# Optimization experiments

Measured on AMD Instinct MI355X. Metric: run time of the kernel, lower is better.

## Reference

```python
import jax, jax.numpy as jnp
import numpy as np

B, T, S, D, H, DK = 2, 2048, 2048, 1024, 16, 64


def setup_inputs() -> dict:
    key = jax.random.key(0)
    ks = jax.random.split(key, 11)
    s = 1.0 / np.sqrt(D)
    return {
        "query": jax.random.normal(ks[0], (B, T, D), jnp.float32),
        "value": jax.random.normal(ks[1], (B, S, D), jnp.float32),
        "key": jax.random.normal(ks[2], (B, S, D), jnp.float32),
        "Wq": jax.random.normal(ks[3], (D, H, DK), jnp.float32) * s,
        "bq": jnp.zeros((H, DK), jnp.float32),
        "Wk": jax.random.normal(ks[4], (D, H, DK), jnp.float32) * s,
        "bk": jnp.zeros((H, DK), jnp.float32),
        "Wv": jax.random.normal(ks[5], (D, H, DK), jnp.float32) * s,
        "bv": jnp.zeros((H, DK), jnp.float32),
        "Wo": jax.random.normal(ks[6], (H, DK, D), jnp.float32) * (1.0 / np.sqrt(H * DK)),
        "bo": jnp.zeros((D,), jnp.float32),
    }


def reference(query, value, key, Wq, bq, Wk, bk, Wv, bv, Wo, bo):
    # Projections: (B, seq, D) x (D, H, DK) -> (B, seq, H, DK)
    q = jnp.einsum("btd,dhk->bthk", query, Wq) + bq
    k = jnp.einsum("bsd,dhk->bshk", key, Wk) + bk
    v = jnp.einsum("bsd,dhk->bshk", value, Wv) + bv
    # Scaled dot-product attention (keras scales query by 1/sqrt(key_dim))
    q = q * (1.0 / np.sqrt(DK)).astype(np.float32)
    scores = jnp.einsum("bshk,bthk->bhts", k, q)  # (B, H, T, S)
    probs = jax.nn.softmax(scores, axis=-1)
    attn = jnp.einsum("bhts,bshk->bthk", probs, v)  # (B, T, H, DK)
    # Output projection back to model dim
    out = jnp.einsum("bthk,hkd->btd", attn, Wo) + bo
    return out
```

## Files before the change

kernel.cpp:

```cpp
#include <hip/hip_runtime.h>
#include <math.h>

#define BB  2
#define TT  2048
#define SSQ 2048
#define DD  1024
#define HH  16
#define DKK 64
#define MM  (BB*TT)
#define NN  (HH*DKK)

typedef __attribute__((ext_vector_type(8))) short short8;
typedef __attribute__((ext_vector_type(4))) float f32x4;
typedef __attribute__((ext_vector_type(2))) unsigned int uint2v;
typedef __attribute__((ext_vector_type(4))) unsigned int u32x4;

__device__ __forceinline__ short f2bf(float x) {
    unsigned u = __builtin_bit_cast(unsigned, x);
    unsigned r = (u + 0x7FFFu + ((u >> 16) & 1u)) >> 16;
    return (short)r;
}

__device__ __forceinline__ unsigned pk2(float lo, float hi) {
    return (__builtin_bit_cast(unsigned, hi) & 0xFFFF0000u) |
           (__builtin_bit_cast(unsigned, lo) >> 16);
}

__device__ __forceinline__ short8 cvt8(f32x4 x, f32x4 y) {
    unsigned r0, r1, r2, r3;
    asm("v_cvt_pk_bf16_f32 %0, %1, %2" : "=v"(r0) : "v"(x[0]), "v"(x[1]));
    asm("v_cvt_pk_bf16_f32 %0, %1, %2" : "=v"(r1) : "v"(x[2]), "v"(x[3]));
    asm("v_cvt_pk_bf16_f32 %0, %1, %2" : "=v"(r2) : "v"(y[0]), "v"(y[1]));
    asm("v_cvt_pk_bf16_f32 %0, %1, %2" : "=v"(r3) : "v"(y[2]), "v"(y[3]));
    u32x4 r;
    r[0] = r0; r[1] = r1; r[2] = r2; r[3] = r3;
    return __builtin_bit_cast(short8, r);
}

__device__ __forceinline__ void glds16(const void* g, void* l) {
    __builtin_amdgcn_global_load_lds(
        (const __attribute__((address_space(1))) void*)g,
        (__attribute__((address_space(3))) void*)l, 16, 0, 0);
}

__global__ __launch_bounds__(256)
void wtrans(const float* __restrict__ w0, const float* __restrict__ w1,
            const float* __restrict__ w2, const float* __restrict__ w3,
            short* __restrict__ t0, short* __restrict__ t1,
            short* __restrict__ t2, short* __restrict__ t3)
{
    __shared__ float Ls[64][65];
    int z = blockIdx.z;
    const float* in = (z == 0) ? w0 : (z == 1) ? w1 : (z == 2) ? w2 : w3;
    short* out = (z == 0) ? t0 : (z == 1) ? t1 : (z == 2) ? t2 : t3;
    const int r0 = blockIdx.y * 64, c0 = blockIdx.x * 64;
    const int t = threadIdx.x;
    const int r = t >> 2, c4 = t & 3;

    const float* src = in + (size_t)(r0 + r) * DD + c0 + c4 * 16;
#pragma unroll
    for (int i = 0; i < 4; i++) {
        f32x4 f = *(const f32x4*)(src + i * 4);
#pragma unroll
        for (int j = 0; j < 4; j++) Ls[r][c4 * 16 + i * 4 + j] = f[j];
    }
    __syncthreads();

    short8 va, vb;
#pragma unroll
    for (int j = 0; j < 8; j++) va[j] = f2bf(Ls[c4 * 16 + j][r]);
#pragma unroll
    for (int j = 0; j < 8; j++) vb[j] = f2bf(Ls[c4 * 16 + 8 + j][r]);
    short* dst = out + (size_t)(c0 + r) * DD + r0 + c4 * 16;
    *(short8*)dst = va;
    *(short8*)(dst + 8) = vb;
}

__global__ __launch_bounds__(256, 3)
void gemm_qkv(const float* __restrict__ Aqf, const float* __restrict__ Akf,
              const float* __restrict__ Avf,
              const short* __restrict__ Wqt, const short* __restrict__ Wkt,
              const short* __restrict__ Wvt,
              const float* __restrict__ bq, const float* __restrict__ bk,
              const float* __restrict__ bv,
              short* __restrict__ Qb, short* __restrict__ Kb,
              short* __restrict__ Vbt)
{
    __shared__ short As[2][128 * 32];
    __shared__ short Bs[2][128 * 32];

    const int d = blockIdx.x + 8 * blockIdx.y + 256 * blockIdx.z;
    const int kx = d & 7, j = d >> 3;
    const int z = j >> 5;
    const int n0 = ((j >> 2) & 7) * 128;
    const int m0 = (4 * kx + (j & 3)) * 128;

    const float* A  = (z == 0) ? Aqf : (z == 1) ? Akf : Avf;
    const short* Bt = (z == 0) ? Wqt : (z == 1) ? Wkt : Wvt;
    const float* bias = (z == 0) ? bq : (z == 1) ? bk : bv;

    const int tid = threadIdx.x;
    const int w = tid >> 6, l = tid & 63;
    const int l15 = l & 15, quad = l >> 4;
    const int wm = w >> 1, wn = w & 1;
    const int r = tid >> 2, cseg = tid & 3;

    f32x4 acc[4][4];
#pragma unroll
    for (int i = 0; i < 4; i++)
#pragma unroll
        for (int jj = 0; jj < 4; jj++) acc[i][jj] = (f32x4){0.f, 0.f, 0.f, 0.f};

    const float* gA0 = A + (size_t)(m0 + r) * DD + cseg * 8;
    const float* gA1 = gA0 + (size_t)64 * DD;
    const short* gB  = Bt + (size_t)(n0 + r) * DD + cseg * 8;
    const int aoff0 = r * 32 + cseg * 8;
    const int aoff1 = (64 + r) * 32 + cseg * 8;

    glds16(gB + 0,                &Bs[0][w * 512]);
    glds16(gB + (size_t)64 * DD,  &Bs[0][2048 + w * 512]);
    {
        f32x4 a00 = *(const f32x4*)(gA0);
        f32x4 a01 = *(const f32x4*)(gA0 + 4);
        f32x4 a10 = *(const f32x4*)(gA1);
        f32x4 a11 = *(const f32x4*)(gA1 + 4);
        *(short8*)&As[0][aoff0] = cvt8(a00, a01);
        *(short8*)&As[0][aoff1] = cvt8(a10, a11);
    }

    for (int k0 = 0; k0 < DD; k0 += 32) {
        const int cur = (k0 >> 5) & 1;
        __syncthreads();
        const bool more = (k0 + 32) < DD;
        f32x4 a00, a01, a10, a11;
        if (more) {
            glds16(gB + k0 + 32,                  &Bs[cur ^ 1][w * 512]);
            glds16(gB + (size_t)64 * DD + k0 + 32, &Bs[cur ^ 1][2048 + w * 512]);
            a00 = *(const f32x4*)(gA0 + k0 + 32);
            a01 = *(const f32x4*)(gA0 + k0 + 36);
            a10 = *(const f32x4*)(gA1 + k0 + 32);
            a11 = *(const f32x4*)(gA1 + k0 + 36);
        }

        short8 bF[4];
#pragma unroll
        for (int ni = 0; ni < 4; ni++)
            bF[ni] = *(const short8*)&Bs[cur][(wn * 64 + ni * 16 + l15) * 32 + quad * 8];
        if (z != 2) {
#pragma unroll
            for (int mi = 0; mi < 4; mi++) {
                short8 aF = *(const short8*)&As[cur][(wm * 64 + mi * 16 + l15) * 32 + quad * 8];
#pragma unroll
                for (int ni = 0; ni < 4; ni++)
                    acc[mi][ni] = __builtin_amdgcn_mfma_f32_16x16x32_bf16(aF, bF[ni], acc[mi][ni], 0, 0, 0);
            }
        } else {
#pragma unroll
            for (int mi = 0; mi < 4; mi++) {
                short8 aF = *(const short8*)&As[cur][(wm * 64 + mi * 16 + l15) * 32 + quad * 8];
#pragma unroll
                for (int ni = 0; ni < 4; ni++)
                    acc[ni][mi] = __builtin_amdgcn_mfma_f32_16x16x32_bf16(bF[ni], aF, acc[ni][mi], 0, 0, 0);
            }
        }

        if (more) {
            *(short8*)&As[cur ^ 1][aoff0] = cvt8(a00, a01);
            *(short8*)&As[cur ^ 1][aoff1] = cvt8(a10, a11);
        }
    }

    if (z != 2) {
        short* dst = (z == 0) ? Qb : Kb;
        const float scale = (z == 0) ? 0.1803368801f : 1.0f;
#pragma unroll
        for (int mi = 0; mi < 4; mi++) {
#pragma unroll
            for (int reg = 0; reg < 4; reg++) {
                int m = m0 + wm * 64 + mi * 16 + quad * 4 + reg;
                int b = m >> 11, t = m & 2047;
#pragma unroll
                for (int ni = 0; ni < 4; ni++) {
                    int n = n0 + wn * 64 + ni * 16 + l15;
                    float vv = (acc[mi][ni][reg] + bias[n]) * scale;
                    int h = n >> 6, dk = n & 63;
                    dst[((size_t)(b * HH + h) * TT + t) * DKK + dk] = f2bf(vv);
                }
            }
        }
    } else {
        const int b = m0 >> 11;
        const int tl0 = (m0 & 2047) + wm * 64;
#pragma unroll
        for (int ni = 0; ni < 4; ni++) {
#pragma unroll
            for (int reg = 0; reg < 4; reg++) {
                int n = n0 + wn * 64 + ni * 16 + quad * 4 + reg;
                int h = n >> 6, dk = n & 63;
                float bb = bias[n];
                short* vrow = Vbt + ((size_t)(b * HH + h) * DKK + dk) * SSQ;
#pragma unroll
                for (int mi = 0; mi < 4; mi++) {
                    int t = tl0 + mi * 16 + l15;
                    vrow[t] = f2bf(acc[ni][mi][reg] + bb);
                }
            }
        }
    }
}

__global__ __launch_bounds__(256, 3)
void gemm_out(const short* __restrict__ Ab, const short* __restrict__ Wot,
              const float* __restrict__ bo, float* __restrict__ out)
{
    __shared__ short As[2][64 * 32];
    __shared__ short Bs[2][128 * 32];

    const int d = blockIdx.x + 8 * blockIdx.y;
    const int kx = d & 7, j = d >> 3;
    const int m0 = (8 * kx + (j & 7)) * 64;
    const int n0 = (j >> 3) * 128;

    const int tid = threadIdx.x;
    const int w = tid >> 6, l = tid & 63;
    const int l15 = l & 15, quad = l >> 4;
    const int wm = w >> 1, wn = w & 1;

    f32x4 acc[2][4];
#pragma unroll
    for (int i = 0; i < 2; i++)
#pragma unroll
        for (int jj = 0; jj < 4; jj++) acc[i][jj] = (f32x4){0.f, 0.f, 0.f, 0.f};

    const int r = tid >> 2, cseg = tid & 3;
    const short* gA = Ab + (size_t)(m0 + r) * DD + cseg * 8;
    const short* gB = Wot + (size_t)(n0 + r) * DD + cseg * 8;

    glds16(gA + 0,               &As[0][w * 512]);
    glds16(gB + 0,               &Bs[0][w * 512]);
    glds16(gB + (size_t)64 * DD, &Bs[0][2048 + w * 512]);

    for (int k0 = 0; k0 < DD; k0 += 32) {
        const int cur = (k0 >> 5) & 1;
        __syncthreads();
        if (k0 + 32 < DD) {
            glds16(gA + k0 + 32,                   &As[cur ^ 1][w * 512]);
            glds16(gB + k0 + 32,                   &Bs[cur ^ 1][w * 512]);
            glds16(gB + (size_t)64 * DD + k0 + 32, &Bs[cur ^ 1][2048 + w * 512]);
        }

        short8 bF[4];
#pragma unroll
        for (int ni = 0; ni < 4; ni++)
            bF[ni] = *(const short8*)&Bs[cur][(wn * 64 + ni * 16 + l15) * 32 + quad * 8];
#pragma unroll
        for (int mi = 0; mi < 2; mi++) {
            short8 aF = *(const short8*)&As[cur][(wm * 32 + mi * 16 + l15) * 32 + quad * 8];
#pragma unroll
            for (int ni = 0; ni < 4; ni++)
                acc[mi][ni] = __builtin_amdgcn_mfma_f32_16x16x32_bf16(aF, bF[ni], acc[mi][ni], 0, 0, 0);
        }
    }

#pragma unroll
    for (int mi = 0; mi < 2; mi++) {
#pragma unroll
        for (int reg = 0; reg < 4; reg++) {
            int m = m0 + wm * 32 + mi * 16 + quad * 4 + reg;
#pragma unroll
            for (int ni = 0; ni < 4; ni++) {
                int n = n0 + wn * 64 + ni * 16 + l15;
                out[(size_t)m * DD + n] = acc[mi][ni][reg] + bo[n];
            }
        }
    }
}

__global__ __launch_bounds__(256, 4)
void attn_mfma(const short* __restrict__ Qb, const short* __restrict__ Kb,
               const short* __restrict__ Vbt,
               float* __restrict__ O1, float* __restrict__ O2,
               float* __restrict__ l1, float* __restrict__ l2)
{
    __shared__ short KV[2 * 2 * 64 * 72];

    const int tid = threadIdx.x;
    const int w = tid >> 6, l = tid & 63;
    const int l15 = l & 15, quad = l >> 4;

    const int fid = blockIdx.y * 16 + blockIdx.x;
    const int swz = (fid & 7) * 64 + (fid >> 3);
    const int t0 = (swz & 15) * 128;
    const int bh = swz >> 4;
    const int half = blockIdx.z;
    const size_t hb = (size_t)bh * SSQ * DKK;
    const int r = tid >> 2, c4 = tid & 3;
    const int sbase = half * 1024;

    short8 qf[2][2];
#pragma unroll
    for (int mf = 0; mf < 2; mf++)
#pragma unroll
        for (int kk = 0; kk < 2; kk++)
            qf[mf][kk] = *(const short8*)(Qb + hb +
                (size_t)(t0 + 32 * w + 16 * mf + l15) * DKK + kk * 32 + quad * 8);

    const short* gkb = Kb + hb + (size_t)(sbase + r) * DKK + c4 * 16;
    const short* gvb = Vbt + hb + (size_t)r * SSQ + sbase + c4 * 16;
    short8 kr0 = *(const short8*)(gkb + 0);
    short8 kr1 = *(const short8*)(gkb + 8);
    short8 vr0 = *(const short8*)(gvb + 0);
    short8 vr1 = *(const short8*)(gvb + 8);

    f32x4 o[2][4];
#pragma unroll
    for (int mf = 0; mf < 2; mf++)
#pragma unroll
        for (int j = 0; j < 4; j++) o[mf][j] = (f32x4){0.f, 0.f, 0.f, 0.f};
    f32x4 lacc[2] = {(f32x4){0.f, 0.f, 0.f, 0.f}, (f32x4){0.f, 0.f, 0.f, 0.f}};
    const short8 ones = {(short)0x3F80, (short)0x3F80, (short)0x3F80, (short)0x3F80,
                         (short)0x3F80, (short)0x3F80, (short)0x3F80, (short)0x3F80};

    short* skb = KV + r * 72 + c4 * 16;

    for (int s0 = 0; s0 < 1024; s0 += 64) {
        const int dbo = (s0 & 64) ? 9216 : 0;
        *(short8*)(skb + dbo)          = kr0;
        *(short8*)(skb + dbo + 8)      = kr1;
        *(short8*)(skb + dbo + 4608)   = vr0;
        *(short8*)(skb + dbo + 4616)   = vr1;
        if (s0 + 64 < 1024) {
            const short* gk = gkb + (size_t)(s0 + 64) * DKK;
            const short* gv = gvb + (s0 + 64);
            kr0 = *(const short8*)(gk + 0);
            kr1 = *(const short8*)(gk + 8);
            vr0 = *(const short8*)(gv + 0);
            vr1 = *(const short8*)(gv + 8);
        }
        __syncthreads();
        const short* kb_ = KV + dbo;
        const short* vb_ = kb_ + 4608;

        f32x4 sc[4][2];
#pragma unroll
        for (int np = 0; np < 4; np++)
#pragma unroll
            for (int mf = 0; mf < 2; mf++) sc[np][mf] = (f32x4){0.f, 0.f, 0.f, 0.f};
        __builtin_amdgcn_s_setprio(1);
#pragma unroll
        for (int kk = 0; kk < 2; kk++) {
#pragma unroll
            for (int np = 0; np < 4; np++) {
                short8 aK = *(const short8*)&kb_[(16 * np + l15) * 72 + kk * 32 + quad * 8];
                sc[np][0] = __builtin_amdgcn_mfma_f32_16x16x32_bf16(aK, qf[0][kk], sc[np][0], 0, 0, 0);
                sc[np][1] = __builtin_amdgcn_mfma_f32_16x16x32_bf16(aK, qf[1][kk], sc[np][1], 0, 0, 0);
            }
        }
        __builtin_amdgcn_s_setprio(0);

        short8 pa[2][2];
#pragma unroll
        for (int mf = 0; mf < 2; mf++) {
#pragma unroll
            for (int kk = 0; kk < 2; kk++) {
                u32x4 wd;
#pragma unroll
                for (int b = 0; b < 2; b++) {
                    float p00 = __builtin_amdgcn_exp2f(sc[2 * kk][mf][2 * b]);
                    float p01 = __builtin_amdgcn_exp2f(sc[2 * kk][mf][2 * b + 1]);
                    float p10 = __builtin_amdgcn_exp2f(sc[2 * kk + 1][mf][2 * b]);
                    float p11 = __builtin_amdgcn_exp2f(sc[2 * kk + 1][mf][2 * b + 1]);
                    unsigned Xw = pk2(p00, p01);
                    unsigned Yw = pk2(p10, p11);
                    uint2v s1 = __builtin_amdgcn_permlane32_swap(Xw, Yw, false, false);
                    uint2v s2 = __builtin_amdgcn_permlane16_swap(s1[0], s1[1], false, false);
                    wd[b]     = s2[0];
                    wd[2 + b] = s2[1];
                }
                pa[mf][kk] = __builtin_bit_cast(short8, wd);
            }
        }

        __builtin_amdgcn_s_setprio(1);
#pragma unroll
        for (int kk = 0; kk < 2; kk++) {
            lacc[0] = __builtin_amdgcn_mfma_f32_16x16x32_bf16(pa[0][kk], ones, lacc[0], 0, 0, 0);
            lacc[1] = __builtin_amdgcn_mfma_f32_16x16x32_bf16(pa[1][kk], ones, lacc[1], 0, 0, 0);
#pragma unroll
            for (int np = 0; np < 4; np++) {
                short8 bV = *(const short8*)&vb_[(16 * np + l15) * 72 + kk * 32 + quad * 8];
                o[0][np] = __builtin_amdgcn_mfma_f32_16x16x32_bf16(pa[0][kk], bV, o[0][np], 0, 0, 0);
                o[1][np] = __builtin_amdgcn_mfma_f32_16x16x32_bf16(pa[1][kk], bV, o[1][np], 0, 0, 0);
            }
        }
        __builtin_amdgcn_s_setprio(0);
    }

    float* O = half ? O2 : O1;
    float* L = half ? l2 : l1;
    const size_t rowb = (size_t)bh * TT;
#pragma unroll
    for (int mf = 0; mf < 2; mf++) {
#pragma unroll
        for (int reg = 0; reg < 4; reg++) {
            int t = t0 + 32 * w + 16 * mf + quad * 4 + reg;
            if (l15 == 0) L[rowb + t] = lacc[mf][reg];
            float* orow = O + (rowb + t) * DKK;
#pragma unroll
            for (int np = 0; np < 4; np++)
                orow[16 * np + l15] = o[mf][np][reg];
        }
    }
}

__global__ __launch_bounds__(256)
void combine_norm(const float* __restrict__ O1, const float* __restrict__ O2,
                  const float* __restrict__ l1, const float* __restrict__ l2,
                  short* __restrict__ Ab)
{
    size_t g = (size_t)blockIdx.x * 256 + threadIdx.x;
    size_t i0 = g * 8;
    int bh = (int)(i0 >> 17);
    int t  = (int)((i0 >> 6) & 2047);
    int dk = (int)(i0 & 63);
    float inv = 1.f / (l1[(size_t)bh * TT + t] + l2[(size_t)bh * TT + t]);
    f32x4 a0 = *(const f32x4*)(O1 + i0);
    f32x4 a1 = *(const f32x4*)(O1 + i0 + 4);
    f32x4 b0 = *(const f32x4*)(O2 + i0);
    f32x4 b1 = *(const f32x4*)(O2 + i0 + 4);
    short8 v;
#pragma unroll
    for (int j = 0; j < 4; j++) v[j] = f2bf((a0[j] + b0[j]) * inv);
#pragma unroll
    for (int j = 0; j < 4; j++) v[4 + j] = f2bf((a1[j] + b1[j]) * inv);
    int b = bh >> 4, h = bh & 15;
    *(short8*)(Ab + (((size_t)(b * TT + t) * HH + h) * DKK + dk)) = v;
}

extern "C" void kernel_launch(void* const* d_in, const int* in_sizes, int n_in,
                              void* d_out, int out_size, void* d_ws, size_t ws_size,
                              hipStream_t stream)
{
    const float* query = (const float*)d_in[0];
    const float* value = (const float*)d_in[1];
    const float* key   = (const float*)d_in[2];
    const float* Wq    = (const float*)d_in[3];
    const float* bq    = (const float*)d_in[4];
    const float* Wk    = (const float*)d_in[5];
    const float* bk    = (const float*)d_in[6];
    const float* Wv    = (const float*)d_in[7];
    const float* bv    = (const float*)d_in[8];
    const float* Wo    = (const float*)d_in[9];
    const float* bo    = (const float*)d_in[10];
    float* out = (float*)d_out;

    const size_t actE = (size_t)MM * DD;
    const size_t wE   = (size_t)DD * NN;
    short* p = (short*)d_ws;
    short* Wqt  = p; p += wE;
    short* Wkt  = p; p += wE;
    short* Wvt  = p; p += wE;
    short* Wot  = p; p += wE;
    short* Qb   = p; p += actE;
    short* Kb   = p; p += actE;
    short* Vbt  = p; p += actE;
    short* Ab   = p; p += actE;
    float* O1f  = (float*)p; p += 2 * actE;
    float* O2f  = (float*)p; p += 2 * actE;
    float* l1f  = (float*)p; p += 4 * (size_t)BB * HH * TT;
    float* l2f  = l1f + (size_t)BB * HH * TT;

    dim3 blk(256);

    wtrans<<<dim3(16, 16, 4), blk, 0, stream>>>(Wq, Wk, Wv, Wo, Wqt, Wkt, Wvt, Wot);

    gemm_qkv<<<dim3(NN / 128, MM / 128, 3), blk, 0, stream>>>(
        query, key, value, Wqt, Wkt, Wvt, bq, bk, bv, Qb, Kb, Vbt);

    attn_mfma<<<dim3(TT / 128, BB * HH, 2), blk, 0, stream>>>(
        Qb, Kb, Vbt, O1f, O2f, l1f, l2f);

    combine_norm<<<dim3((unsigned)(actE / 2048)), blk, 0, stream>>>(
        O1f, O2f, l1f, l2f, Ab);

    gemm_out<<<dim3(NN / 128, MM / 64), blk, 0, stream>>>(Ab, Wot, bo, out);
}
```

Before: 249.1 us.

## Pre-convert activations to bf16 and use async LDS loads in QKV GEMM

Adds a separate kernel that converts query/key/value from fp32 to bf16 ahead of time, so the QKV GEMM can stage its A tiles with global_load_lds instead of register loads plus in-loop conversion. The output GEMM is also changed to stage K=64 per iteration, which halves the number of barriers. Workspace is reorganized so the attention partial buffers alias the bf16 activation buffers once they are no longer needed. The trade-off is an extra pass over the activations (fp32 read plus bf16 write) and an extra launch.

```diff
diff --git a/kernel.cpp b/kernel.cpp
--- a/kernel.cpp
+++ b/kernel.cpp
@@ -26,21 +26,30 @@
            (__builtin_bit_cast(unsigned, lo) >> 16);
 }
 
-__device__ __forceinline__ short8 cvt8(f32x4 x, f32x4 y) {
-    unsigned r0, r1, r2, r3;
-    asm("v_cvt_pk_bf16_f32 %0, %1, %2" : "=v"(r0) : "v"(x[0]), "v"(x[1]));
-    asm("v_cvt_pk_bf16_f32 %0, %1, %2" : "=v"(r1) : "v"(x[2]), "v"(x[3]));
-    asm("v_cvt_pk_bf16_f32 %0, %1, %2" : "=v"(r2) : "v"(y[0]), "v"(y[1]));
-    asm("v_cvt_pk_bf16_f32 %0, %1, %2" : "=v"(r3) : "v"(y[2]), "v"(y[3]));
-    u32x4 r;
-    r[0] = r0; r[1] = r1; r[2] = r2; r[3] = r3;
-    return __builtin_bit_cast(short8, r);
-}
-
 __device__ __forceinline__ void glds16(const void* g, void* l) {
     __builtin_amdgcn_global_load_lds(
         (const __attribute__((address_space(1))) void*)g,
         (__attribute__((address_space(3))) void*)l, 16, 0, 0);
+}
+
+__global__ __launch_bounds__(256)
+void to_bf16_acts(const float* __restrict__ a0, const float* __restrict__ a1,
+                  const float* __restrict__ a2,
+                  short* __restrict__ o0, short* __restrict__ o1,
+                  short* __restrict__ o2)
+{
+    int z = blockIdx.y;
+    const float* in = (z == 0) ? a0 : (z == 1) ? a1 : a2;
+    short* out = (z == 0) ? o0 : (z == 1) ? o1 : o2;
+    size_t i0 = ((size_t)blockIdx.x * 256 + threadIdx.x) * 8;
+    f32x4 f0 = *(const f32x4*)(in + i0);
+    f32x4 f1 = *(const f32x4*)(in + i0 + 4);
+    short8 v;
+#pragma unroll
+    for (int j = 0; j < 4; j++) v[j] = f2bf(f0[j]);
+#pragma unroll
+    for (int j = 0; j < 4; j++) v[4 + j] = f2bf(f1[j]);
+    *(short8*)(out + i0) = v;
 }
 
 __global__ __launch_bounds__(256)
@@ -77,8 +86,8 @@
 }
 
 __global__ __launch_bounds__(256, 3)
-void gemm_qkv(const float* __restrict__ Aqf, const float* __restrict__ Akf,
-              const float* __restrict__ Avf,
+void gemm_qkv(const short* __restrict__ Aq, const short* __restrict__ Ak,
+              const short* __restrict__ Av,
               const short* __restrict__ Wqt, const short* __restrict__ Wkt,
               const short* __restrict__ Wvt,
               const float* __restrict__ bq, const float* __restrict__ bk,
@@ -95,7 +104,7 @@
     const int n0 = ((j >> 2) & 7) * 128;
     const int m0 = (4 * kx + (j & 3)) * 128;
 
-    const float* A  = (z == 0) ? Aqf : (z == 1) ? Akf : Avf;
+    const short* A  = (z == 0) ? Aq : (z == 1) ? Ak : Av;
     const short* Bt = (z == 0) ? Wqt : (z == 1) ? Wkt : Wvt;
     const float* bias = (z == 0) ? bq : (z == 1) ? bk : bv;
 
@@ -111,35 +120,22 @@
 #pragma unroll
         for (int jj = 0; jj < 4; jj++) acc[i][jj] = (f32x4){0.f, 0.f, 0.f, 0.f};
 
-    const float* gA0 = A + (size_t)(m0 + r) * DD + cseg * 8;
-    const float* gA1 = gA0 + (size_t)64 * DD;
-    const short* gB  = Bt + (size_t)(n0 + r) * DD + cseg * 8;
-    const int aoff0 = r * 32 + cseg * 8;
-    const int aoff1 = (64 + r) * 32 + cseg * 8;
-
-    glds16(gB + 0,                &Bs[0][w * 512]);
-    glds16(gB + (size_t)64 * DD,  &Bs[0][2048 + w * 512]);
-    {
-        f32x4 a00 = *(const f32x4*)(gA0);
-        f32x4 a01 = *(const f32x4*)(gA0 + 4);
-        f32x4 a10 = *(const f32x4*)(gA1);
-        f32x4 a11 = *(const f32x4*)(gA1 + 4);
-        *(short8*)&As[0][aoff0] = cvt8(a00, a01);
-        *(short8*)&As[0][aoff1] = cvt8(a10, a11);
-    }
+    const short* gA = A + (size_t)(m0 + r) * DD + cseg * 8;
+    const short* gB = Bt + (size_t)(n0 + r) * DD + cseg * 8;
+
+    glds16(gA + 0,               &As[0][w * 512]);
+    glds16(gA + (size_t)64 * DD, &As[0][2048 + w * 512]);
+    glds16(gB + 0,               &Bs[0][w * 512]);
+    glds16(gB + (size_t)64 * DD, &Bs[0][2048 + w * 512]);
 
     for (int k0 = 0; k0 < DD; k0 += 32) {
         const int cur = (k0 >> 5) & 1;
         __syncthreads();
-        const bool more = (k0 + 32) < DD;
-        f32x4 a00, a01, a10, a11;
-        if (more) {
-            glds16(gB + k0 + 32,                  &Bs[cur ^ 1][w * 512]);
+        if (k0 + 32 < DD) {
+            glds16(gA + k0 + 32,                   &As[cur ^ 1][w * 512]);
+            glds16(gA + (size_t)64 * DD + k0 + 32, &As[cur ^ 1][2048 + w * 512]);
+            glds16(gB + k0 + 32,                   &Bs[cur ^ 1][w * 512]);
             glds16(gB + (size_t)64 * DD + k0 + 32, &Bs[cur ^ 1][2048 + w * 512]);
-            a00 = *(const f32x4*)(gA0 + k0 + 32);
-            a01 = *(const f32x4*)(gA0 + k0 + 36);
-            a10 = *(const f32x4*)(gA1 + k0 + 32);
-            a11 = *(const f32x4*)(gA1 + k0 + 36);
         }
 
         short8 bF[4];
@@ -162,11 +158,6 @@
                 for (int ni = 0; ni < 4; ni++)
                     acc[ni][mi] = __builtin_amdgcn_mfma_f32_16x16x32_bf16(bF[ni], aF, acc[ni][mi], 0, 0, 0);
             }
-        }
-
-        if (more) {
-            *(short8*)&As[cur ^ 1][aoff0] = cvt8(a00, a01);
-            *(short8*)&As[cur ^ 1][aoff1] = cvt8(a10, a11);
         }
     }
 
@@ -213,8 +204,8 @@
 void gemm_out(const short* __restrict__ Ab, const short* __restrict__ Wot,
               const float* __restrict__ bo, float* __restrict__ out)
 {
-    __shared__ short As[2][64 * 32];
-    __shared__ short Bs[2][128 * 32];
+    __shared__ short As[2][2 * 64 * 32];
+    __shared__ short Bs[2][2 * 128 * 32];
 
     const int d = blockIdx.x + 8 * blockIdx.y;
     const int kx = d & 7, j = d >> 3;
@@ -236,31 +227,39 @@
     const short* gA = Ab + (size_t)(m0 + r) * DD + cseg * 8;
     const short* gB = Wot + (size_t)(n0 + r) * DD + cseg * 8;
 
-    glds16(gA + 0,               &As[0][w * 512]);
-    glds16(gB + 0,               &Bs[0][w * 512]);
-    glds16(gB + (size_t)64 * DD, &Bs[0][2048 + w * 512]);
-
-    for (int k0 = 0; k0 < DD; k0 += 32) {
-        const int cur = (k0 >> 5) & 1;
+#define STAGE_OUT(buf, k0)                                                     \
+    do {                                                                       \
+        glds16(gA + (k0),                        &As[buf][w * 512]);           \
+        glds16(gA + (k0) + 32,                   &As[buf][2048 + w * 512]);    \
+        glds16(gB + (k0),                        &Bs[buf][w * 512]);           \
+        glds16(gB + (size_t)64 * DD + (k0),      &Bs[buf][2048 + w * 512]);    \
+        glds16(gB + (k0) + 32,                   &Bs[buf][4096 + w * 512]);    \
+        glds16(gB + (size_t)64 * DD + (k0) + 32, &Bs[buf][6144 + w * 512]);    \
+    } while (0)
+
+    STAGE_OUT(0, 0);
+
+    for (int k0 = 0; k0 < DD; k0 += 64) {
+        const int cur = (k0 >> 6) & 1;
         __syncthreads();
-        if (k0 + 32 < DD) {
-            glds16(gA + k0 + 32,                   &As[cur ^ 1][w * 512]);
-            glds16(gB + k0 + 32,                   &Bs[cur ^ 1][w * 512]);
-            glds16(gB + (size_t)64 * DD + k0 + 32, &Bs[cur ^ 1][2048 + w * 512]);
-        }
-
-        short8 bF[4];
-#pragma unroll
-        for (int ni = 0; ni < 4; ni++)
-            bF[ni] = *(const short8*)&Bs[cur][(wn * 64 + ni * 16 + l15) * 32 + quad * 8];
-#pragma unroll
-        for (int mi = 0; mi < 2; mi++) {
-            short8 aF = *(const short8*)&As[cur][(wm * 32 + mi * 16 + l15) * 32 + quad * 8];
+        if (k0 + 64 < DD) STAGE_OUT(cur ^ 1, k0 + 64);
+
+#pragma unroll
+        for (int kk = 0; kk < 2; kk++) {
+            short8 bF[4];
 #pragma unroll
             for (int ni = 0; ni < 4; ni++)
-                acc[mi][ni] = __builtin_amdgcn_mfma_f32_16x16x32_bf16(aF, bF[ni], acc[mi][ni], 0, 0, 0);
-        }
-    }
+                bF[ni] = *(const short8*)&Bs[cur][kk * 4096 + (wn * 64 + ni * 16 + l15) * 32 + quad * 8];
+#pragma unroll
+            for (int mi = 0; mi < 2; mi++) {
+                short8 aF = *(const short8*)&As[cur][kk * 2048 + (wm * 32 + mi * 16 + l15) * 32 + quad * 8];
+#pragma unroll
+                for (int ni = 0; ni < 4; ni++)
+                    acc[mi][ni] = __builtin_amdgcn_mfma_f32_16x16x32_bf16(aF, bF[ni], acc[mi][ni], 0, 0, 0);
+            }
+        }
+    }
+#undef STAGE_OUT
 
 #pragma unroll
     for (int mi = 0; mi < 2; mi++) {
@@ -457,6 +456,9 @@
     const size_t actE = (size_t)MM * DD;
     const size_t wE   = (size_t)DD * NN;
     short* p = (short*)d_ws;
+    short* Aq   = p; p += actE;
+    short* Ak   = p; p += actE;
+    short* Av   = p; p += actE;
     short* Wqt  = p; p += wE;
     short* Wkt  = p; p += wE;
     short* Wvt  = p; p += wE;
@@ -465,17 +467,20 @@
     short* Kb   = p; p += actE;
     short* Vbt  = p; p += actE;
     short* Ab   = p; p += actE;
-    float* O1f  = (float*)p; p += 2 * actE;
     float* O2f  = (float*)p; p += 2 * actE;
-    float* l1f  = (float*)p; p += 4 * (size_t)BB * HH * TT;
+    float* O1f  = (float*)Aq;
+    float* l1f  = (float*)Av;
     float* l2f  = l1f + (size_t)BB * HH * TT;
 
     dim3 blk(256);
 
+    to_bf16_acts<<<dim3((unsigned)(actE / 2048), 3), blk, 0, stream>>>(
+        query, key, value, Aq, Ak, Av);
+
     wtrans<<<dim3(16, 16, 4), blk, 0, stream>>>(Wq, Wk, Wv, Wo, Wqt, Wkt, Wvt, Wot);
 
     gemm_qkv<<<dim3(NN / 128, MM / 128, 3), blk, 0, stream>>>(
-        query, key, value, Wqt, Wkt, Wvt, bq, bk, bv, Qb, Kb, Vbt);
+        Aq, Ak, Av, Wqt, Wkt, Wvt, bq, bk, bv, Qb, Kb, Vbt);
 
     attn_mfma<<<dim3(TT / 128, BB * HH, 2), blk, 0, stream>>>(
         Qb, Kb, Vbt, O1f, O2f, l1f, l2f);
```

New measurement: 225.4 us. 9.5% less time.
